# Optimization experiments

Measured on AMD Instinct MI355X. Metric: run time of the kernel, lower is better.

The kernel has to match this reference:

```python
import jax, jax.numpy as jnp
import numpy as np
import math

NEG = -1000000.0


def setup_inputs() -> dict:
    key = jax.random.key(0)
    ks = jax.random.split(key, 8)
    B, S, D = 4, 2048, 1024
    std = 1.0 / math.sqrt(D)
    return {
        "queries": jax.random.normal(ks[0], (B, S, D), jnp.float32),
        "keys": jax.random.normal(ks[1], (B, S, D), jnp.float32),
        "values": jax.random.normal(ks[2], (B, S, D), jnp.float32),
        "valid_len": jax.random.randint(ks[3], (B,), 1, S, dtype=jnp.int64 if jax.config.jax_enable_x64 else jnp.int32),
        "W_q": jax.random.normal(ks[4], (D, D), jnp.float32) * std,
        "W_k": jax.random.normal(ks[5], (D, D), jnp.float32) * std,
        "W_v": jax.random.normal(ks[6], (D, D), jnp.float32) * std,
        "W_o": jax.random.normal(ks[7], (D, D), jnp.float32) * std,
    }


def reference(queries, keys, values, valid_len, W_q, W_k, W_v, W_o):
    NUM_HEADS = 16
    B, S, D = queries.shape
    hd = D // NUM_HEADS

    def split_heads(x):
        # (B, S, D) -> (B, H, S, hd)
        return x.reshape(B, -1, NUM_HEADS, hd).transpose(0, 2, 1, 3)

    # nn.Linear with weight W applies x @ W.T
    q = split_heads(queries @ W_q.T)
    k = split_heads(keys @ W_k.T)
    v = split_heads(values @ W_v.T)

    scale = 1.0 / math.sqrt(hd)
    scores = jnp.einsum('bhqd,bhkd->bhqk', q, k) * scale  # (B, H, Sq, Sk)

    # key-padding mask from valid_len: positions >= valid_len are masked
    kpos = jnp.arange(scores.shape[-1])
    pad_mask = kpos[None, None, None, :] >= valid_len[:, None, None, None]
    scores = jnp.where(pad_mask, NEG, scores)
    attn = jax.nn.softmax(scores, axis=-1)

    out = jnp.einsum('bhqk,bhkd->bhqd', attn, v)  # (B, H, Sq, hd)
    out = out.transpose(0, 2, 1, 3).reshape(B, -1, D)
    return out @ W_o.T
```

## Files before the change

### kernel.cpp

```cpp
#include <hip/hip_runtime.h>
#include <hip/hip_bf16.h>

using bf16_t = __bf16;
using bf16x8 = __attribute__((ext_vector_type(8))) __bf16;
using bf16x4 = __attribute__((ext_vector_type(4))) __bf16;
using f32x4  = __attribute__((ext_vector_type(4))) float;

#define S_  2048
#define D_  1024

typedef __attribute__((address_space(1))) unsigned int glb_u32;
typedef __attribute__((address_space(3))) unsigned int lds_u32;

__device__ __forceinline__ void async_cp16(const void* g, void* lds) {
    __builtin_amdgcn_global_load_lds(
        (glb_u32*)(unsigned long long)g,
        (lds_u32*)(unsigned int)(unsigned long long)lds,
        16, 0, 0);
}

__global__ __launch_bounds__(256) void cast7(const float* __restrict__ q, const float* __restrict__ k,
                                             const float* __restrict__ v, const float* __restrict__ Wq,
                                             const float* __restrict__ Wk, const float* __restrict__ Wv,
                                             const float* __restrict__ Wo,
                                             bf16_t* __restrict__ oq, bf16_t* __restrict__ ok,
                                             bf16_t* __restrict__ ov, bf16_t* __restrict__ oWq,
                                             bf16_t* __restrict__ oWk, bf16_t* __restrict__ oWv,
                                             bf16_t* __restrict__ oWo) {
    int y = blockIdx.y;
    int i = blockIdx.x * 256 + threadIdx.x;
    const float* s; bf16_t* d; int n4;
    if      (y == 0) { s = q;  d = oq;  n4 = 2097152; }
    else if (y == 1) { s = k;  d = ok;  n4 = 2097152; }
    else if (y == 2) { s = v;  d = ov;  n4 = 2097152; }
    else if (y == 3) { s = Wq; d = oWq; n4 = 262144;  }
    else if (y == 4) { s = Wk; d = oWk; n4 = 262144;  }
    else if (y == 5) { s = Wv; d = oWv; n4 = 262144;  }
    else             { s = Wo; d = oWo; n4 = 262144;  }
    if (i >= n4) return;
    float4 f = reinterpret_cast<const float4*>(s)[i];
    bf16x4 o;
    o[0] = (bf16_t)f.x; o[1] = (bf16_t)f.y; o[2] = (bf16_t)f.z; o[3] = (bf16_t)f.w;
    reinterpret_cast<bf16x4*>(d)[i] = o;
}

__global__ __launch_bounds__(256) void cast4_f32_bf16(const float* __restrict__ a, const float* __restrict__ b,
                                                      const float* __restrict__ c, const float* __restrict__ dd,
                                                      bf16_t* __restrict__ oa, bf16_t* __restrict__ ob,
                                                      bf16_t* __restrict__ oc, bf16_t* __restrict__ od, int n4) {
    int i = blockIdx.x * 256 + threadIdx.x;
    if (i >= n4) return;
    const float* s; bf16_t* d;
    int w = blockIdx.y;
    if      (w == 0) { s = a;  d = oa; }
    else if (w == 1) { s = b;  d = ob; }
    else if (w == 2) { s = c;  d = oc; }
    else             { s = dd; d = od; }
    float4 f = reinterpret_cast<const float4*>(s)[i];
    bf16x4 o;
    o[0] = (bf16_t)f.x; o[1] = (bf16_t)f.y; o[2] = (bf16_t)f.z; o[3] = (bf16_t)f.w;
    reinterpret_cast<bf16x4*>(d)[i] = o;
}

template <int MODE>
__global__ __launch_bounds__(512, 2) void gemm8(const bf16_t* __restrict__ Aq,
                                                const bf16_t* __restrict__ Ak,
                                                const bf16_t* __restrict__ Av,
                                                const bf16_t* __restrict__ Wq,
                                                const bf16_t* __restrict__ Wk,
                                                const bf16_t* __restrict__ Wv,
                                                bf16_t* __restrict__ Qp,
                                                bf16_t* __restrict__ Kp,
                                                bf16_t* __restrict__ Vt,
                                                float cs,
                                                float* __restrict__ Co) {
    __shared__ bf16_t As[2][2][128 * 32];
    __shared__ bf16_t Bs[2][2][256 * 32];
    const int K = 1024;
    constexpr int NKT = 16;
    int tid  = threadIdx.x;
    int lane = tid & 63, w = tid >> 6;
    int l15  = lane & 15, quad = lane >> 4;
    int wr = w >> 2, wc = w & 3;

    int bid = blockIdx.x;
    int xcd = bid & 7, r = bid >> 3;
    int z = 0, r2 = r;
    if (MODE == 0) { z = r >> 5; r2 = r & 31; }
    int m0 = (xcd * 8 + (r2 & 7)) * 128;
    int n0 = (r2 >> 3) * 256;

    const bf16_t *Ag, *Bg;
    if (MODE == 0) {
        Ag = (z == 0) ? Aq : (z == 1) ? Ak : Av;
        Bg = (z == 0) ? Wq : (z == 1) ? Wk : Wv;
    } else { Ag = Aq; Bg = Wq; }

    const bf16_t* aS; const bf16_t* bS[2]; int bOff[2];
    {
        int row = tid >> 2, s = tid & 3;
        aS = Ag + (size_t)(m0 + row) * K + ((s ^ ((row >> 1) & 3)) * 8);
    }
#pragma unroll
    for (int j = 0; j < 2; j++) {
        int c = j * 512 + tid;
        int row = c >> 2, s = c & 3;
        bS[j] = Bg + (size_t)(n0 + row) * K + ((s ^ ((row >> 1) & 3)) * 8);
        bOff[j] = c * 8;
    }
    auto stage = [&](int buf, int t, int kh) {
        int koff = t * 64 + kh * 32;
        async_cp16(aS + koff,    &As[buf][kh][tid * 8]);
        async_cp16(bS[0] + koff, &Bs[buf][kh][bOff[0]]);
        async_cp16(bS[1] + koff, &Bs[buf][kh][bOff[1]]);
    };

    int aoff[4], boff[4];
#pragma unroll
    for (int i = 0; i < 4; i++) {
        int row = wr * 64 + i * 16 + l15;
        aoff[i] = row * 32 + ((quad ^ ((row >> 1) & 3)) * 8);
    }
#pragma unroll
    for (int jn = 0; jn < 4; jn++) {
        int row = wc * 64 + jn * 16 + l15;
        boff[jn] = row * 32 + ((quad ^ ((row >> 1) & 3)) * 8);
    }

    f32x4 acc[4][4] = {};

    stage(0, 0, 0);
    stage(0, 0, 1);
    asm volatile("s_waitcnt vmcnt(3)" ::: "memory");
    __builtin_amdgcn_s_barrier();

    for (int t = 0; t < NKT; ++t) {
        int buf = t & 1, nbuf = buf ^ 1;
        bool st = (t + 1 < NKT);
        bf16x8 af[4], bfr[4];

#pragma unroll
        for (int kh = 0; kh < 2; kh++) {
            const bf16_t* Ah = As[buf][kh];
            const bf16_t* Bh = Bs[buf][kh];
#pragma unroll
            for (int i = 0; i < 4; i++)  af[i]  = *reinterpret_cast<const bf16x8*>(&Ah[aoff[i]]);
#pragma unroll
            for (int jn = 0; jn < 4; jn++) bfr[jn] = *reinterpret_cast<const bf16x8*>(&Bh[boff[jn]]);
            if (st) stage(nbuf, t + 1, kh);
            __builtin_amdgcn_s_barrier();
            asm volatile("s_waitcnt lgkmcnt(0)" ::: "memory");
            __builtin_amdgcn_sched_barrier(0);
            __builtin_amdgcn_s_setprio(1);
#pragma unroll
            for (int i = 0; i < 4; i++)
#pragma unroll
                for (int jn = 0; jn < 4; jn++)
                    acc[i][jn] = __builtin_amdgcn_mfma_f32_16x16x32_bf16(af[i], bfr[jn], acc[i][jn], 0, 0, 0);
            __builtin_amdgcn_s_setprio(0);
            if (t == NKT - 1) asm volatile("s_waitcnt vmcnt(0)" ::: "memory");
            else              asm volatile("s_waitcnt vmcnt(3)" ::: "memory");
            __builtin_amdgcn_s_barrier();
        }
    }

    if (MODE == 0 && z == 2) {
#pragma unroll
        for (int i = 0; i < 4; i++)
#pragma unroll
            for (int jn = 0; jn < 4; jn++) {
                int m = m0 + wr * 64 + i * 16 + quad * 4;
                int n = n0 + wc * 64 + jn * 16 + l15;
                bf16x4 o4;
#pragma unroll
                for (int rr = 0; rr < 4; rr++) o4[rr] = (bf16_t)acc[i][jn][rr];
                size_t vrow = (size_t)((m >> 11) * 16 + (n >> 6)) * 64 + (n & 63);
                int ml = m & 2047;
                int mp = (ml & ~31) | (((ml >> 2) & 3) << 3) | (((ml >> 4) & 1) << 2);
                *reinterpret_cast<bf16x4*>(&Vt[vrow * S_ + mp]) = o4;
            }
    } else if (MODE == 0) {
        bf16_t* CoH = (z == 0) ? Qp : Kp;
        float scale = (z == 0) ? cs : 1.0f;
#pragma unroll
        for (int i = 0; i < 4; i++)
#pragma unroll
            for (int jn = 0; jn < 4; jn++)
#pragma unroll
                for (int rr = 0; rr < 4; rr++) {
                    int m = m0 + wr * 64 + i * 16 + quad * 4 + rr;
                    int n = n0 + wc * 64 + jn * 16 + l15;
                    CoH[(size_t)m * 1024 + n] = (bf16_t)(acc[i][jn][rr] * scale);
                }
    } else {
#pragma unroll
        for (int i = 0; i < 4; i++)
#pragma unroll
            for (int jn = 0; jn < 4; jn++)
#pragma unroll
                for (int rr = 0; rr < 4; rr++) {
                    int m = m0 + wr * 64 + i * 16 + quad * 4 + rr;
                    int n = n0 + wc * 64 + jn * 16 + l15;
                    Co[(size_t)m * 1024 + n] = acc[i][jn][rr];
                }
    }
}

__global__ __launch_bounds__(256, 4) void qkv_gemm(const float* __restrict__ qf,
                                                   const float* __restrict__ kf,
                                                   const float* __restrict__ vf,
                                                   const bf16_t* __restrict__ Wqb,
                                                   const bf16_t* __restrict__ Wkb,
                                                   const bf16_t* __restrict__ Wvb,
                                                   bf16_t* __restrict__ Qp,
                                                   bf16_t* __restrict__ Kp,
                                                   bf16_t* __restrict__ Vt,
                                                   float cs) {
    __shared__ bf16_t As[2][128 * 32];
    __shared__ bf16_t Bs[3][128 * 32];
    const int K = 1024;
    int tid  = threadIdx.x;
    int lane = tid & 63;
    int w    = tid >> 6;
    int l15  = lane & 15, quad = lane >> 4;

    int bid = blockIdx.x;
    int xcd = bid & 7, idx = bid >> 3;
    int z   = idx >> 6;
    int rem = idx & 63;
    int m0 = (xcd * 8 + (rem & 7)) * 128;
    int n0 = (rem >> 3) * 128;
    int wm = (w >> 1) * 64, wn = (w & 1) * 64;

    const float*  Af; const bf16_t* Bt;
    if      (z == 0) { Af = qf; Bt = Wqb; }
    else if (z == 1) { Af = kf; Bt = Wkb; }
    else             { Af = vf; Bt = Wvb; }
    float scale = (z == 0) ? cs : 1.0f;

    const float* Ag = Af + (size_t)(m0 + (tid >> 2)) * K + (tid & 3) * 8;
    int arow = tid >> 2, aslot = tid & 3;
    int aoff = arow * 32 + ((aslot ^ ((arow >> 1) & 3)) * 8);

    const bf16_t* bSrc[2]; int bOff[2];
#pragma unroll
    for (int j = 0; j < 2; j++) {
        int linear = j * 256 + tid;
        int row = linear >> 2, s = linear & 3;
        bSrc[j] = Bt + (size_t)(n0 + row) * K + ((s ^ ((row >> 1) & 3)) * 8);
        bOff[j] = linear * 8;
    }

    float4 aE[4], aO[4];
    auto loadA = [&](float4* a, int k0) {
        const float* p = Ag + k0;
        a[0] = *reinterpret_cast<const float4*>(p);
        a[1] = *reinterpret_cast<const float4*>(p + 4);
        a[2] = *reinterpret_cast<const float4*>(p + (size_t)64 * K);
        a[3] = *reinterpret_cast<const float4*>(p + (size_t)64 * K + 4);
    };
    auto storeA = [&](bf16_t* dst, const float4* a) {
        bf16x8 o0, o1;
        o0[0] = (bf16_t)a[0].x; o0[1] = (bf16_t)a[0].y; o0[2] = (bf16_t)a[0].z; o0[3] = (bf16_t)a[0].w;
        o0[4] = (bf16_t)a[1].x; o0[5] = (bf16_t)a[1].y; o0[6] = (bf16_t)a[1].z; o0[7] = (bf16_t)a[1].w;
        o1[0] = (bf16_t)a[2].x; o1[1] = (bf16_t)a[2].y; o1[2] = (bf16_t)a[2].z; o1[3] = (bf16_t)a[2].w;
        o1[4] = (bf16_t)a[3].x; o1[5] = (bf16_t)a[3].y; o1[6] = (bf16_t)a[3].z; o1[7] = (bf16_t)a[3].w;
        *reinterpret_cast<bf16x8*>(dst + aoff)        = o0;
        *reinterpret_cast<bf16x8*>(dst + aoff + 2048) = o1;
    };
    auto stageB = [&](bf16_t* dst, int k0) {
        async_cp16(bSrc[0] + k0, dst + bOff[0]);
        async_cp16(bSrc[1] + k0, dst + bOff[1]);
    };

    f32x4 acc[4][4] = {};
    bf16_t *bRead = Bs[0], *bMid = Bs[1], *bStage = Bs[2];

    loadA(aE, 0);
    stageB(Bs[0], 0);
    loadA(aO, 32);
    stageB(Bs[1], 32);
    storeA(As[0], aE);
    asm volatile("s_waitcnt vmcnt(6) lgkmcnt(0)" ::: "memory");
    __builtin_amdgcn_s_barrier();

#pragma unroll 2
    for (int i = 0; i < 32; ++i) {
        int k2 = (i + 2 < 32) ? (i + 2) * 32 : 992;
        float4* aNew = (i & 1) ? aO : aE;
        loadA(aNew, k2);
        stageB(bStage, k2);

        const bf16_t* Ac = As[i & 1];
        bf16x8 af[4], bfr[4];
#pragma unroll
        for (int t = 0; t < 4; t++) {
            int ra = wm + t * 16 + l15;
            int rb = wn + t * 16 + l15;
            af[t]  = *reinterpret_cast<const bf16x8*>(&Ac[ra * 32 + ((quad ^ ((ra >> 1) & 3)) * 8)]);
            bfr[t] = *reinterpret_cast<const bf16x8*>(&bRead[rb * 32 + ((quad ^ ((rb >> 1) & 3)) * 8)]);
        }
#pragma unroll
        for (int mt = 0; mt < 4; mt++)
#pragma unroll
            for (int nt = 0; nt < 4; nt++)
                acc[mt][nt] = __builtin_amdgcn_mfma_f32_16x16x32_bf16(af[mt], bfr[nt], acc[mt][nt], 0, 0, 0);

        if (i + 1 < 32) storeA(As[(i + 1) & 1], (i & 1) ? aE : aO);

        bf16_t* t0 = bRead; bRead = bMid; bMid = bStage; bStage = t0;
        asm volatile("s_waitcnt vmcnt(6) lgkmcnt(0)" ::: "memory");
        __builtin_amdgcn_s_barrier();
    }

    if (z == 2) {
#pragma unroll
        for (int mt = 0; mt < 4; mt++)
#pragma unroll
            for (int nt = 0; nt < 4; nt++) {
                int m = m0 + wm + mt * 16 + quad * 4;
                int n = n0 + wn + nt * 16 + l15;
                bf16x4 o4;
#pragma unroll
                for (int r = 0; r < 4; r++) o4[r] = (bf16_t)acc[mt][nt][r];
                size_t vrow = (size_t)((m >> 11) * 16 + (n >> 6)) * 64 + (n & 63);
                int ml = m & 2047;
                int mp = (ml & ~31) | (((ml >> 2) & 3) << 3) | (((ml >> 4) & 1) << 2);
                *reinterpret_cast<bf16x4*>(&Vt[vrow * S_ + mp]) = o4;
            }
    } else {
        bf16_t* Co = (z == 0) ? Qp : Kp;
#pragma unroll
        for (int mt = 0; mt < 4; mt++)
#pragma unroll
            for (int nt = 0; nt < 4; nt++)
#pragma unroll
                for (int r = 0; r < 4; r++) {
                    int m = m0 + wm + mt * 16 + quad * 4 + r;
                    int n = n0 + wn + nt * 16 + l15;
                    Co[(size_t)m * 1024 + n] = (bf16_t)(acc[mt][nt][r] * scale);
                }
    }
}

__global__ __launch_bounds__(256) void attn_fused(const bf16_t* __restrict__ Qp,
                                                  const bf16_t* __restrict__ Kp,
                                                  const bf16_t* __restrict__ Vt,
                                                  const int* __restrict__ vlen_p,
                                                  bf16_t* __restrict__ Out) {
    __shared__ bf16_t smem[4][64 * 64];

    int tid  = threadIdx.x;
    int lane = tid & 63, w = tid >> 6;
    int l15  = lane & 15, quad = lane >> 4;

    int nk[4], ord[4] = {0, 1, 2, 3};
#pragma unroll
    for (int i = 0; i < 4; i++) nk[i] = (vlen_p[i] + 63) >> 6;
#pragma unroll
    for (int i = 0; i < 3; i++)
#pragma unroll
        for (int j = 0; j < 3 - i; j++)
            if (nk[ord[j + 1]] > nk[ord[j]]) { int t = ord[j]; ord[j] = ord[j + 1]; ord[j + 1] = t; }

    int bid  = blockIdx.x;
    int b    = ord[bid >> 9];
    int t    = bid & 511;
    int h    = (t & 7) * 2 + ((t >> 3) & 1);
    int qblk = t >> 4;
    int vlen = vlen_p[b];
    int nkb  = (vlen + 63) >> 6;

    const bf16_t* Qg = Qp + (size_t)(b * S_ + qblk * 64) * D_ + h * 64;
    const bf16_t* Kg = Kp + (size_t)b * S_ * D_ + h * 64;
    const bf16_t* Vg = Vt + (size_t)(b * 16 + h) * 64 * S_;

    int r0 = tid >> 3, s0 = tid & 7;
    int sx = (s0 ^ (r0 & 7)) * 8;
    const bf16_t* kS0 = Kg + (size_t)r0 * D_ + sx;
    const bf16_t* kS1 = kS0 + (size_t)32 * D_;
    const bf16_t* vS0 = Vg + (size_t)r0 * S_ + sx;
    const bf16_t* vS1 = vS0 + (size_t)32 * S_;

    {
        const bf16_t* qS0 = Qg + (size_t)r0 * D_ + sx;
        async_cp16(qS0,                   smem[2] + tid * 8);
        async_cp16(qS0 + (size_t)32 * D_, smem[2] + tid * 8 + 2048);
        async_cp16(kS0, smem[0] + tid * 8);
        async_cp16(kS1, smem[0] + tid * 8 + 2048);
        async_cp16(vS0, smem[1] + tid * 8);
        async_cp16(vS1, smem[1] + tid * 8 + 2048);
    }
    __syncthreads();

    bf16x8 qf[2];
    {
        int row = w * 16 + l15, x = row & 7;
#pragma unroll
        for (int kk = 0; kk < 2; kk++)
            qf[kk] = *reinterpret_cast<const bf16x8*>(&smem[2][row * 64 + ((kk * 4 + quad) ^ x) * 8]);
    }
    __syncthreads();

    f32x4 o[4] = {};
    float l_st = 0.f;

    for (int kb = 0; kb < nkb; kb++) {
        int cur = kb & 1;
        if (kb + 1 < nkb) {
            int nxt = cur ^ 1;
            kS0 += (size_t)64 * D_; kS1 += (size_t)64 * D_;
            vS0 += 64;              vS1 += 64;
            async_cp16(kS0, smem[nxt * 2]     + tid * 8);
            async_cp16(kS1, smem[nxt * 2]     + tid * 8 + 2048);
            async_cp16(vS0, smem[nxt * 2 + 1] + tid * 8);
            async_cp16(vS1, smem[nxt * 2 + 1] + tid * 8 + 2048);
        }
        const bf16_t* Kc = smem[cur * 2];
        const bf16_t* Vc = smem[cur * 2 + 1];

        f32x4 sc[4] = {};
#pragma unroll
        for (int nt = 0; nt < 4; nt++) {
            int row = nt * 16 + l15, x = row & 7;
#pragma unroll
            for (int kk = 0; kk < 2; kk++) {
                bf16x8 kf = *reinterpret_cast<const bf16x8*>(&Kc[row * 64 + ((kk * 4 + quad) ^ x) * 8]);
                sc[nt] = __builtin_amdgcn_mfma_f32_16x16x32_bf16(kf, qf[kk], sc[nt], 0, 0, 0);
            }
        }

        bool partial = (vlen & 63) && (kb == nkb - 1);
        bf16x8 pf[2];
        float lacc = 0.f;
        if (!partial) {
#pragma unroll
            for (int nt = 0; nt < 4; nt++)
#pragma unroll
                for (int r = 0; r < 4; r++) {
                    float p = __builtin_exp2f(sc[nt][r]);
                    lacc += p;
                    pf[nt >> 1][(nt & 1) * 4 + r] = (bf16_t)p;
                }
        } else {
#pragma unroll
            for (int nt = 0; nt < 4; nt++)
#pragma unroll
                for (int r = 0; r < 4; r++) {
                    float p = __builtin_exp2f(sc[nt][r]);
                    if (kb * 64 + nt * 16 + quad * 4 + r >= vlen) p = 0.f;
                    lacc += p;
                    pf[nt >> 1][(nt & 1) * 4 + r] = (bf16_t)p;
                }
        }
        l_st += lacc;

#pragma unroll
        for (int np = 0; np < 2; np++)
#pragma unroll
            for (int dt = 0; dt < 4; dt++) {
                int row = dt * 16 + l15, x = row & 7;
                bf16x8 vfr = *reinterpret_cast<const bf16x8*>(&Vc[row * 64 + ((np * 4 + quad) ^ x) * 8]);
                o[dt] = __builtin_amdgcn_mfma_f32_16x16x32_bf16(vfr, pf[np], o[dt], 0, 0, 0);
            }

        __syncthreads();
    }

    float l = l_st;
    l += __shfl_xor(l, 16);
    l += __shfl_xor(l, 32);
    float inv = 1.0f / l;

    bf16_t* T = smem[0];
    {
        int row = w * 16 + l15, x = row & 7;
#pragma unroll
        for (int dt = 0; dt < 4; dt++) {
            bf16x4 o4;
#pragma unroll
            for (int r = 0; r < 4; r++) o4[r] = (bf16_t)(o[dt][r] * inv);
            int slot = dt * 2 + (quad >> 1);
            *reinterpret_cast<bf16x4*>(&T[row * 64 + (slot ^ x) * 8 + (quad & 1) * 4]) = o4;
        }
    }
    __syncthreads();
    {
        int row = tid >> 2, ch = tid & 3, x = row & 7;
        size_t obase = (size_t)(b * S_ + qblk * 64 + row) * D_ + h * 64 + ch * 16;
        bf16x8 f0 = *reinterpret_cast<const bf16x8*>(&T[row * 64 + ((ch * 2)     ^ x) * 8]);
        bf16x8 f1 = *reinterpret_cast<const bf16x8*>(&T[row * 64 + ((ch * 2 + 1) ^ x) * 8]);
        *reinterpret_cast<bf16x8*>(&Out[obase])     = f0;
        *reinterpret_cast<bf16x8*>(&Out[obase + 8]) = f1;
    }
}

__global__ __launch_bounds__(256) void gemm_out(const bf16_t* __restrict__ A,
                                                const bf16_t* __restrict__ Bt,
                                                float* __restrict__ C) {
    __shared__ bf16_t As[3][128 * 32];
    __shared__ bf16_t Bs[3][128 * 32];
    const int K = 1024;
    int tid  = threadIdx.x;
    int lane = tid & 63;
    int w    = tid >> 6;
    int l15  = lane & 15, quad = lane >> 4;

    int bid = blockIdx.x;
    int xcd = bid & 7, idx = bid >> 3;
    int m0 = (xcd * 8 + (idx & 7)) * 128;
    int n0 = (idx >> 3) * 128;
    int wm = (w >> 1) * 64, wn = (w & 1) * 64;

    const bf16_t* aSrc[2]; const bf16_t* bSrc[2];
    int dOff[2];
#pragma unroll
    for (int j = 0; j < 2; j++) {
        int linear = j * 256 + tid;
        int row = linear >> 2, s = linear & 3;
        int sw = (s ^ ((row >> 1) & 3)) * 8;
        aSrc[j] = A  + (size_t)(m0 + row) * K + sw;
        bSrc[j] = Bt + (size_t)(n0 + row) * K + sw;
        dOff[j] = linear * 8;
    }

    auto stage = [&](int buf, int koff) {
#pragma unroll
        for (int j = 0; j < 2; j++) async_cp16(aSrc[j] + koff, &As[buf][dOff[j]]);
#pragma unroll
        for (int j = 0; j < 2; j++) async_cp16(bSrc[j] + koff, &Bs[buf][dOff[j]]);
    };

    f32x4 acc[4][4] = {};

    stage(0, 0);
    stage(1, 32);

    int cur = 0, nx2 = 2;
    for (int i = 0; i < 32; ++i) {
        if (i == 31) asm volatile("s_waitcnt vmcnt(0)" ::: "memory");
        else         asm volatile("s_waitcnt vmcnt(4)" ::: "memory");
        __builtin_amdgcn_s_barrier();
        if (i + 2 < 32) stage(nx2, (i + 2) * 32);

        bf16x8 af[4], bfr[4];
#pragma unroll
        for (int t = 0; t < 4; t++) {
            int ra = wm + t * 16 + l15;
            int rb = wn + t * 16 + l15;
            af[t]  = *reinterpret_cast<const bf16x8*>(&As[cur][ra * 32 + ((quad ^ ((ra >> 1) & 3)) * 8)]);
            bfr[t] = *reinterpret_cast<const bf16x8*>(&Bs[cur][rb * 32 + ((quad ^ ((rb >> 1) & 3)) * 8)]);
        }
#pragma unroll
        for (int mt = 0; mt < 4; mt++)
#pragma unroll
            for (int nt = 0; nt < 4; nt++)
                acc[mt][nt] = __builtin_amdgcn_mfma_f32_16x16x32_bf16(af[mt], bfr[nt], acc[mt][nt], 0, 0, 0);

        cur = (cur == 2) ? 0 : cur + 1;
        nx2 = (nx2 == 2) ? 0 : nx2 + 1;
    }

#pragma unroll
    for (int mt = 0; mt < 4; mt++)
#pragma unroll
        for (int nt = 0; nt < 4; nt++)
#pragma unroll
            for (int r = 0; r < 4; r++) {
                int m = m0 + wm + mt * 16 + quad * 4 + r;
                int n = n0 + wn + nt * 16 + l15;
                C[(size_t)m * 1024 + n] = acc[mt][nt][r];
            }
}

extern "C" void kernel_launch(void* const* d_in, const int* in_sizes, int n_in,
                              void* d_out, int out_size, void* d_ws, size_t ws_size,
                              hipStream_t stream) {
    const float* q  = (const float*)d_in[0];
    const float* k  = (const float*)d_in[1];
    const float* v  = (const float*)d_in[2];
    const int*   vl = (const int*)d_in[3];
    const float* Wq = (const float*)d_in[4];
    const float* Wk = (const float*)d_in[5];
    const float* Wv = (const float*)d_in[6];
    const float* Wo = (const float*)d_in[7];
    float* out = (float*)d_out;

    bf16_t* ws = (bf16_t*)d_ws;
    const size_t SD = (size_t)8192 * 1024;
    const size_t WW = (size_t)1024 * 1024;
    const float cs = 0.18033688f;
    dim3 blk(256);

    size_t need = (6 * SD + 4 * WW) * sizeof(bf16_t);
    if (ws_size >= need) {
        bf16_t* qb  = ws;
        bf16_t* kb  = ws + SD;
        bf16_t* vb  = ws + 2 * SD;
        bf16_t* Qp  = ws + 3 * SD;
        bf16_t* Kp  = ws + 4 * SD;
        bf16_t* Vt  = ws + 5 * SD;
        bf16_t* Wqb = ws + 6 * SD;
        bf16_t* Wkb = Wqb + WW;
        bf16_t* Wvb = Wqb + 2 * WW;
        bf16_t* Wob = Wqb + 3 * WW;

        cast7<<<dim3(8192, 7), blk, 0, stream>>>(q, k, v, Wq, Wk, Wv, Wo,
                                                 qb, kb, vb, Wqb, Wkb, Wvb, Wob);
        gemm8<0><<<dim3(768), dim3(512), 0, stream>>>(qb, kb, vb, Wqb, Wkb, Wvb, Qp, Kp, Vt, cs, nullptr);
        attn_fused<<<dim3(2048), blk, 0, stream>>>(Qp, Kp, Vt, vl, qb);
        gemm8<1><<<dim3(256), dim3(512), 0, stream>>>(qb, nullptr, nullptr, Wob, nullptr, nullptr,
                                                      nullptr, nullptr, nullptr, 1.0f, out);
    } else {
        bf16_t* tmpB = ws + SD;
        bf16_t* Qp   = ws + 2 * SD;
        bf16_t* Kp   = ws + 3 * SD;
        bf16_t* Vt   = ws + 4 * SD;
        bf16_t* Wqb  = ws + 5 * SD;
        bf16_t* Wkb  = Wqb + WW;
        bf16_t* Wvb  = Wqb + 2 * WW;
        bf16_t* Wob  = Wqb + 3 * WW;

        cast4_f32_bf16<<<dim3(1024, 4), blk, 0, stream>>>(Wq, Wk, Wv, Wo, Wqb, Wkb, Wvb, Wob, 262144);
        qkv_gemm<<<dim3(1536), blk, 0, stream>>>(q, k, v, Wqb, Wkb, Wvb, Qp, Kp, Vt, cs);
        attn_fused<<<dim3(2048), blk, 0, stream>>>(Qp, Kp, Vt, vl, tmpB);
        gemm_out<<<dim3(512), blk, 0, stream>>>(tmpB, Wob, out);
    }
}
```

Baseline: 317.8 us.

## Deepen GEMM pipeline to 5-stage ring and compute softmax row sums via MFMA

```diff
diff --git a/kernel.cpp b/kernel.cpp
--- a/kernel.cpp
+++ b/kernel.cpp
@@ -74,10 +74,10 @@
                                                 bf16_t* __restrict__ Vt,
                                                 float cs,
                                                 float* __restrict__ Co) {
-    __shared__ bf16_t As[2][2][128 * 32];
-    __shared__ bf16_t Bs[2][2][256 * 32];
+    __shared__ bf16_t As[5][128 * 32];
+    __shared__ bf16_t Bs[5][256 * 32];
     const int K = 1024;
-    constexpr int NKT = 16;
+    constexpr int NKT = 32;
     int tid  = threadIdx.x;
     int lane = tid & 63, w = tid >> 6;
     int l15  = lane & 15, quad = lane >> 4;
@@ -108,11 +108,11 @@
         bS[j] = Bg + (size_t)(n0 + row) * K + ((s ^ ((row >> 1) & 3)) * 8);
         bOff[j] = c * 8;
     }
-    auto stage = [&](int buf, int t, int kh) {
-        int koff = t * 64 + kh * 32;
-        async_cp16(aS + koff,    &As[buf][kh][tid * 8]);
-        async_cp16(bS[0] + koff, &Bs[buf][kh][bOff[0]]);
-        async_cp16(bS[1] + koff, &Bs[buf][kh][bOff[1]]);
+    auto stage = [&](int buf, int t) {
+        int koff = t * 32;
+        async_cp16(aS + koff,    &As[buf][tid * 8]);
+        async_cp16(bS[0] + koff, &Bs[buf][bOff[0]]);
+        async_cp16(bS[1] + koff, &Bs[buf][bOff[1]]);
     };
 
     int aoff[4], boff[4];
@@ -129,39 +129,35 @@
 
     f32x4 acc[4][4] = {};
 
-    stage(0, 0, 0);
-    stage(0, 0, 1);
-    asm volatile("s_waitcnt vmcnt(3)" ::: "memory");
+    stage(0, 0); stage(1, 1); stage(2, 2); stage(3, 3);
+    asm volatile("s_waitcnt vmcnt(9)" ::: "memory");
     __builtin_amdgcn_s_barrier();
 
+    int cur = 0, st4 = 4;
     for (int t = 0; t < NKT; ++t) {
-        int buf = t & 1, nbuf = buf ^ 1;
-        bool st = (t + 1 < NKT);
+        int tn = (t + 4 < NKT) ? t + 4 : NKT - 1;
+        const bf16_t* Ah = As[cur];
+        const bf16_t* Bh = Bs[cur];
         bf16x8 af[4], bfr[4];
-
-#pragma unroll
-        for (int kh = 0; kh < 2; kh++) {
-            const bf16_t* Ah = As[buf][kh];
-            const bf16_t* Bh = Bs[buf][kh];
-#pragma unroll
-            for (int i = 0; i < 4; i++)  af[i]  = *reinterpret_cast<const bf16x8*>(&Ah[aoff[i]]);
-#pragma unroll
-            for (int jn = 0; jn < 4; jn++) bfr[jn] = *reinterpret_cast<const bf16x8*>(&Bh[boff[jn]]);
-            if (st) stage(nbuf, t + 1, kh);
-            __builtin_amdgcn_s_barrier();
-            asm volatile("s_waitcnt lgkmcnt(0)" ::: "memory");
-            __builtin_amdgcn_sched_barrier(0);
-            __builtin_amdgcn_s_setprio(1);
-#pragma unroll
-            for (int i = 0; i < 4; i++)
-#pragma unroll
-                for (int jn = 0; jn < 4; jn++)
-                    acc[i][jn] = __builtin_amdgcn_mfma_f32_16x16x32_bf16(af[i], bfr[jn], acc[i][jn], 0, 0, 0);
-            __builtin_amdgcn_s_setprio(0);
-            if (t == NKT - 1) asm volatile("s_waitcnt vmcnt(0)" ::: "memory");
-            else              asm volatile("s_waitcnt vmcnt(3)" ::: "memory");
-            __builtin_amdgcn_s_barrier();
-        }
+#pragma unroll
+        for (int i = 0; i < 4; i++)  af[i]  = *reinterpret_cast<const bf16x8*>(&Ah[aoff[i]]);
+#pragma unroll
+        for (int jn = 0; jn < 4; jn++) bfr[jn] = *reinterpret_cast<const bf16x8*>(&Bh[boff[jn]]);
+        stage(st4, tn);
+        __builtin_amdgcn_s_barrier();
+        asm volatile("s_waitcnt lgkmcnt(0)" ::: "memory");
+        __builtin_amdgcn_sched_barrier(0);
+        __builtin_amdgcn_s_setprio(1);
+#pragma unroll
+        for (int i = 0; i < 4; i++)
+#pragma unroll
+            for (int jn = 0; jn < 4; jn++)
+                acc[i][jn] = __builtin_amdgcn_mfma_f32_16x16x32_bf16(af[i], bfr[jn], acc[i][jn], 0, 0, 0);
+        __builtin_amdgcn_s_setprio(0);
+        asm volatile("s_waitcnt vmcnt(9)" ::: "memory");
+        __builtin_amdgcn_s_barrier();
+        cur = (cur == 4) ? 0 : cur + 1;
+        st4 = (st4 == 4) ? 0 : st4 + 1;
     }
 
     if (MODE == 0 && z == 2) {
@@ -402,8 +398,12 @@
     }
     __syncthreads();
 
+    bf16x8 ones8;
+#pragma unroll
+    for (int j = 0; j < 8; j++) ones8[j] = (bf16_t)1.0f;
+
     f32x4 o[4] = {};
-    float l_st = 0.f;
+    f32x4 ol = {};
 
     for (int kb = 0; kb < nkb; kb++) {
         int cur = kb & 1;
@@ -432,14 +432,12 @@
 
         bool partial = (vlen & 63) && (kb == nkb - 1);
         bf16x8 pf[2];
-        float lacc = 0.f;
         if (!partial) {
 #pragma unroll
             for (int nt = 0; nt < 4; nt++)
 #pragma unroll
                 for (int r = 0; r < 4; r++) {
                     float p = __builtin_exp2f(sc[nt][r]);
-                    lacc += p;
                     pf[nt >> 1][(nt & 1) * 4 + r] = (bf16_t)p;
                 }
         } else {
@@ -449,11 +447,12 @@
                 for (int r = 0; r < 4; r++) {
                     float p = __builtin_exp2f(sc[nt][r]);
                     if (kb * 64 + nt * 16 + quad * 4 + r >= vlen) p = 0.f;
-                    lacc += p;
                     pf[nt >> 1][(nt & 1) * 4 + r] = (bf16_t)p;
                 }
         }
-        l_st += lacc;
+
+        ol = __builtin_amdgcn_mfma_f32_16x16x32_bf16(ones8, pf[0], ol, 0, 0, 0);
+        ol = __builtin_amdgcn_mfma_f32_16x16x32_bf16(ones8, pf[1], ol, 0, 0, 0);
 
 #pragma unroll
         for (int np = 0; np < 2; np++)
@@ -467,10 +466,7 @@
         __syncthreads();
     }
 
-    float l = l_st;
-    l += __shfl_xor(l, 16);
-    l += __shfl_xor(l, 32);
-    float inv = 1.0f / l;
+    float inv = 1.0f / ol[0];
 
     bf16_t* T = smem[0];
     {
```

New measurement: 307.2 us. 1.03x faster.
